# Kernel tuning notes

Hardware: AMD Instinct MI355X
Metric: run time of the kernel (lower is better)

Reference implementation:

```python
import jax, jax.numpy as jnp
import numpy as np

NEG_SLOPE = 0.01  # torch F.leaky_relu default
N_USER = 100000
N_ITEM = 100000
N_EDGE = 640000
D = 128
N_LAYERS = 3  # 1 input + num_hidden_layers(1) + 1 output layer


def setup_inputs() -> dict:
    key = jax.random.key(0)
    ks = jax.random.split(key, 10)
    scale = 1.0 / np.sqrt(D)
    return {
        "h_user": jax.random.normal(ks[0], (N_USER, D), dtype=jnp.float32),
        "h_item": jax.random.normal(ks[1], (N_ITEM, D), dtype=jnp.float32),
        # W[layer, etype] : etype 0 = user-follows->user, 1 = user-clicks->item, 2 = item-clicked_by->user
        "W": jax.random.normal(ks[2], (N_LAYERS, 3, D, D), dtype=jnp.float32) * scale,
        "b": jnp.zeros((N_LAYERS, 3, D), dtype=jnp.float32),
        "follows_src": jax.random.randint(ks[3], (N_EDGE,), 0, N_USER, dtype=jnp.int32),
        "follows_dst": jax.random.randint(ks[4], (N_EDGE,), 0, N_USER, dtype=jnp.int32),
        "clicks_src": jax.random.randint(ks[5], (N_EDGE,), 0, N_USER, dtype=jnp.int32),
        "clicks_dst": jax.random.randint(ks[6], (N_EDGE,), 0, N_ITEM, dtype=jnp.int32),
        "cb_src": jax.random.randint(ks[7], (N_EDGE,), 0, N_ITEM, dtype=jnp.int32),
        "cb_dst": jax.random.randint(ks[8], (N_EDGE,), 0, N_USER, dtype=jnp.int32),
    }


def _etype_conv(h_src, W, b, src, dst, n_dst):
    """Per-etype Linear on src nodes, copy_u gather, mean-aggregate at dst."""
    Wh = h_src @ W + b                     # [N_src, D] dense transform (once per node)
    msg = Wh[src]                          # [E, D] gather
    s = jax.ops.segment_sum(msg, dst, num_segments=n_dst)
    cnt = jax.ops.segment_sum(jnp.ones((src.shape[0],), dtype=Wh.dtype), dst, num_segments=n_dst)
    return s / jnp.maximum(cnt, 1.0)[:, None]  # mean; isolated nodes -> 0


def _rgcn_forward(h_user, h_item, W, b, follows_src, follows_dst,
                  clicks_src, clicks_dst, cb_src, cb_dst):
    hu, hi = h_user, h_item
    for l in range(N_LAYERS):
        # per-etype mean aggregation, then cross-etype 'sum' (DGL multi_update_all)
        agg_u = (_etype_conv(hu, W[l, 0], b[l, 0], follows_src, follows_dst, N_USER)
                 + _etype_conv(hi, W[l, 2], b[l, 2], cb_src, cb_dst, N_USER))
        agg_i = _etype_conv(hu, W[l, 1], b[l, 1], clicks_src, clicks_dst, N_ITEM)
        hu = jax.nn.leaky_relu(agg_u, NEG_SLOPE)
        hi = jax.nn.leaky_relu(agg_i, NEG_SLOPE)
    return jnp.stack([hu, hi])  # [2, 100000, 128]


def reference(h_user, h_item, W, b, follows_src, follows_dst,
              clicks_src, clicks_dst, cb_src, cb_dst):
    return _rgcn_forward(h_user, h_item, W, b, follows_src, follows_dst,
                         clicks_src, clicks_dst, cb_src, cb_dst)
```

## Files before the change

kernel.cpp:

```cpp
#include <hip/hip_runtime.h>

typedef unsigned short u16;
typedef _Float16 f16;
typedef __attribute__((ext_vector_type(4))) _Float16 f16x4;
typedef __attribute__((ext_vector_type(8))) _Float16 f16x8;
typedef __attribute__((ext_vector_type(4))) float f32x4;

#define D 128

__global__ __launch_bounds__(256) void k_pre(
    const float* __restrict__ h_user, const float* __restrict__ h_item,
    const float* __restrict__ W,
    const int* __restrict__ fd, const int* __restrict__ cd,
    const int* __restrict__ cbd,
    u16* __restrict__ h_all, u16* __restrict__ Wtg,
    int* __restrict__ cnt, u16* __restrict__ pos,
    int NU, int NI, int nf, int nc, int ncb, int S,
    int nbCnt, int nbCvtU, int nbCvtI) {
  int b = blockIdx.x;
  if (b < nbCnt) {
    int e = b * 256 + threadIdx.x;
    int d;
    if (e < nf)
      d = fd[e];
    else if (e < nf + nc)
      d = NU + cd[e - nf];
    else if (e < nf + nc + ncb)
      d = NU + NI + cbd[e - nf - nc];
    else
      return;
    int p = atomicAdd(&cnt[d * S], 1);
    pos[e] = (u16)p;
  } else if (b < nbCnt + nbCvtU + nbCvtI) {
    bool isU = b < nbCnt + nbCvtU;
    int i = (b - (isU ? nbCnt : nbCnt + nbCvtU)) * 256 + threadIdx.x;
    int n8 = (isU ? NU : NI) * 16;
    if (i >= n8) return;
    const float4* ip = (const float4*)(isU ? h_user : h_item);
    u16* op = h_all + (isU ? 0 : (size_t)NU * D);
    float4 a = ip[i * 2], c = ip[i * 2 + 1];
    f16x8 v = {(f16)a.x, (f16)a.y, (f16)a.z, (f16)a.w,
               (f16)c.x, (f16)c.y, (f16)c.z, (f16)c.w};
    *(f16x8*)(op + (size_t)i * 8) = v;
  } else {
    int idx = (b - nbCnt - nbCvtU - nbCvtI) * 256 + threadIdx.x;
    if (idx >= 9 * 16384) return;
    int mat = idx >> 14;
    int k = (idx >> 7) & 127;
    int n = idx & 127;
    ((f16*)Wtg)[(size_t)mat * 16384 + n * 128 + k] = (f16)W[idx];
  }
}

__global__ __launch_bounds__(256) void k_scanA(const int* __restrict__ cnt,
                                               int* __restrict__ part, int n, int S) {
  int t = threadIdx.x;
  int idx = blockIdx.x * 1024 + t * 4;
  int s = 0;
#pragma unroll
  for (int j = 0; j < 4; ++j)
    if (idx + j < n) s += cnt[(idx + j) * S];
  for (int off = 1; off < 64; off <<= 1) s += __shfl_down(s, off, 64);
  __shared__ int ws[4];
  if ((t & 63) == 0) ws[t >> 6] = s;
  __syncthreads();
  if (t == 0) part[blockIdx.x] = ws[0] + ws[1] + ws[2] + ws[3];
}

__global__ __launch_bounds__(1024) void k_scanB(int* __restrict__ part, int n_part) {
  __shared__ int sh[1024];
  int t = threadIdx.x;
  int v = (t < n_part) ? part[t] : 0;
  sh[t] = v;
  __syncthreads();
  for (int off = 1; off < 1024; off <<= 1) {
    int u = (t >= off) ? sh[t - off] : 0;
    __syncthreads();
    sh[t] += u;
    __syncthreads();
  }
  if (t < n_part) part[t] = sh[t] - v;
}

__global__ __launch_bounds__(256) void k_scanC(const int* __restrict__ cnt,
                                               const int* __restrict__ part,
                                               int* __restrict__ rs,
                                               int n, int total, int S) {
  int t = threadIdx.x;
  int idx = blockIdx.x * 1024 + t * 4;
  int v0 = 0, v1 = 0, v2 = 0, v3 = 0;
  if (idx < n) v0 = cnt[idx * S];
  if (idx + 1 < n) v1 = cnt[(idx + 1) * S];
  if (idx + 2 < n) v2 = cnt[(idx + 2) * S];
  if (idx + 3 < n) v3 = cnt[(idx + 3) * S];
  int s = v0 + v1 + v2 + v3;
  int inc = s;
  int lane = t & 63, w = t >> 6;
  for (int off = 1; off < 64; off <<= 1) {
    int u = __shfl_up(inc, off, 64);
    if (lane >= off) inc += u;
  }
  __shared__ int ws[4];
  if (lane == 63) ws[w] = inc;
  __syncthreads();
  int woff = 0;
  for (int i = 0; i < w; ++i) woff += ws[i];
  int ex = part[blockIdx.x] + woff + inc - s;
  int4 r;
  r.x = ex;
  r.y = ex + v0;
  r.z = r.y + v1;
  r.w = r.z + v2;
  if (idx + 3 < n)
    *(int4*)(rs + idx) = r;
  else {
    if (idx < n) rs[idx] = r.x;
    if (idx + 1 < n) rs[idx + 1] = r.y;
    if (idx + 2 < n) rs[idx + 2] = r.z;
    if (idx + 3 < n) rs[idx + 3] = r.w;
  }
  if (blockIdx.x == 0 && t == 0) rs[n] = total;
}

__global__ __launch_bounds__(256) void k_fillpos(
    const int* __restrict__ fs, const int* __restrict__ fd,
    const int* __restrict__ cs, const int* __restrict__ cd,
    const int* __restrict__ cbs, const int* __restrict__ cbd,
    const int* __restrict__ rs, const u16* __restrict__ pos,
    int* __restrict__ csr, int NU, int NI, int nf, int nc, int ncb) {
  int e = blockIdx.x * 256 + threadIdx.x;
  int d, s;
  if (e < nf) {
    d = fd[e];
    s = fs[e];
  } else if (e < nf + nc) {
    d = NU + cd[e - nf];
    s = cs[e - nf];
  } else if (e < nf + nc + ncb) {
    d = NU + NI + cbd[e - nf - nc];
    s = cbs[e - nf - nc] + NU;
  } else
    return;
  csr[rs[d] + (int)pos[e]] = s;
}

__global__ __launch_bounds__(256) void k_agg3(
    const u16* __restrict__ h_all, const int* __restrict__ csr,
    const int* __restrict__ rs, u16* __restrict__ M_all, int N3) {
  int wave = (blockIdx.x * 256 + threadIdx.x) >> 6;
  int lane = threadIdx.x & 63;
  int l16 = lane & 15;
  int w = wave * 4 + (lane >> 4);
  bool valid = w < N3;
  int wc = valid ? w : 0;
  int e = rs[wc];
  int en = valid ? rs[wc + 1] : 0;
  int deg = en - e;
  f16x8 acc0 = {0, 0, 0, 0, 0, 0, 0, 0};
  f16x8 acc1 = {0, 0, 0, 0, 0, 0, 0, 0};
  const char* hb = (const char*)h_all;
  unsigned loff = (unsigned)l16 * 16u;

  while (__any(e < en)) {
    bool a0 = e < en, a1 = e + 1 < en, a2 = e + 2 < en, a3 = e + 3 < en;
    bool a4 = e + 4 < en, a5 = e + 5 < en, a6 = e + 6 < en, a7 = e + 7 < en;
    int s0 = a0 ? csr[e] : 0;
    int s1 = a1 ? csr[e + 1] : 0;
    int s2 = a2 ? csr[e + 2] : 0;
    int s3 = a3 ? csr[e + 3] : 0;
    int s4 = a4 ? csr[e + 4] : 0;
    int s5 = a5 ? csr[e + 5] : 0;
    int s6 = a6 ? csr[e + 6] : 0;
    int s7 = a7 ? csr[e + 7] : 0;
    f16x8 v0 = {0, 0, 0, 0, 0, 0, 0, 0}, v1 = {0, 0, 0, 0, 0, 0, 0, 0};
    f16x8 v2 = {0, 0, 0, 0, 0, 0, 0, 0}, v3 = {0, 0, 0, 0, 0, 0, 0, 0};
    f16x8 v4 = {0, 0, 0, 0, 0, 0, 0, 0}, v5 = {0, 0, 0, 0, 0, 0, 0, 0};
    f16x8 v6 = {0, 0, 0, 0, 0, 0, 0, 0}, v7 = {0, 0, 0, 0, 0, 0, 0, 0};
    if (a0) v0 = *(const f16x8*)(hb + ((unsigned)s0 * 256u + loff));
    if (a1) v1 = *(const f16x8*)(hb + ((unsigned)s1 * 256u + loff));
    if (a2) v2 = *(const f16x8*)(hb + ((unsigned)s2 * 256u + loff));
    if (a3) v3 = *(const f16x8*)(hb + ((unsigned)s3 * 256u + loff));
    if (a4) v4 = *(const f16x8*)(hb + ((unsigned)s4 * 256u + loff));
    if (a5) v5 = *(const f16x8*)(hb + ((unsigned)s5 * 256u + loff));
    if (a6) v6 = *(const f16x8*)(hb + ((unsigned)s6 * 256u + loff));
    if (a7) v7 = *(const f16x8*)(hb + ((unsigned)s7 * 256u + loff));
    acc0 += v0;
    acc1 += v1;
    acc0 += v2;
    acc1 += v3;
    acc0 += v4;
    acc1 += v5;
    acc0 += v6;
    acc1 += v7;
    e += 8;
  }

  if (valid) {
    float invf = deg > 0 ? 1.0f / (float)deg : 0.f;
    f16 hinv = (f16)invf;
    f16x8 t = acc0 + acc1;
    f16x8 r = t * hinv;
    *(f16x8*)((char*)M_all + ((unsigned)wc * 256u + loff)) = r;
  }
}

template <int NE, int OUTF32>
__device__ __forceinline__ void gemm_body(
    const u16* __restrict__ mA, const u16* __restrict__ mBp,
    const u16* __restrict__ wtA, const u16* __restrict__ wtB,
    const float* __restrict__ bA, const float* __restrict__ bB,
    const int* __restrict__ rsA, const int* __restrict__ rsB,
    u16* __restrict__ o16, float* __restrict__ o32, int M, int blk) {
  int tid = threadIdx.x, lane = tid & 63, w = tid >> 6;
  int lr = lane & 15;
  int lk = (lane >> 4) * 8;
  long row0 = (long)blk * 128 + w * 32;

  f32x4 acc[2][8];
#pragma unroll
  for (int rt = 0; rt < 2; rt++)
#pragma unroll
    for (int n = 0; n < 8; n++) acc[rt][n] = (f32x4){0.f, 0.f, 0.f, 0.f};

#pragma unroll
  for (int e = 0; e < NE; ++e) {
    const f16* mm = (const f16*)((e == 0) ? mA : mBp);
    const f16* Wg = (const f16*)((e == 0) ? wtA : wtB);
#pragma unroll
    for (int ks = 0; ks < 4; ++ks) {
      int k0 = ks * 32 + lk;
      f16x8 bf[8];
#pragma unroll
      for (int n = 0; n < 8; n++) bf[n] = *(const f16x8*)(Wg + (n * 16 + lr) * D + k0);
#pragma unroll
      for (int rt = 0; rt < 2; rt++) {
        long r = row0 + rt * 16 + lr;
        if (r >= M) r = M - 1;
        f16x8 af = *(const f16x8*)(mm + r * D + k0);
#pragma unroll
        for (int n = 0; n < 8; n++)
          acc[rt][n] = __builtin_amdgcn_mfma_f32_16x16x32_f16(bf[n], af, acc[rt][n], 0, 0, 0);
      }
    }
  }

  int g4 = (lane >> 4) * 4;
  float4 bAr[8], bBr[8];
#pragma unroll
  for (int n = 0; n < 8; n++) {
    bAr[n] = *(const float4*)&bA[n * 16 + g4];
    if (NE == 2) bBr[n] = *(const float4*)&bB[n * 16 + g4];
  }

#pragma unroll
  for (int rt = 0; rt < 2; rt++) {
    long r = row0 + rt * 16 + lr;
    if (r < M) {
      bool mAok = rsA[r + 1] > rsA[r];
      bool mBok = (NE == 2) && (rsB[r + 1] > rsB[r]);
#pragma unroll
      for (int n = 0; n < 8; n++) {
        float4 vv;
        vv.x = acc[rt][n][0];
        vv.y = acc[rt][n][1];
        vv.z = acc[rt][n][2];
        vv.w = acc[rt][n][3];
        if (mAok) {
          vv.x += bAr[n].x;
          vv.y += bAr[n].y;
          vv.z += bAr[n].z;
          vv.w += bAr[n].w;
        }
        if (mBok) {
          vv.x += bBr[n].x;
          vv.y += bBr[n].y;
          vv.z += bBr[n].z;
          vv.w += bBr[n].w;
        }
        vv.x = vv.x > 0.f ? vv.x : 0.01f * vv.x;
        vv.y = vv.y > 0.f ? vv.y : 0.01f * vv.y;
        vv.z = vv.z > 0.f ? vv.z : 0.01f * vv.z;
        vv.w = vv.w > 0.f ? vv.w : 0.01f * vv.w;
        int col = n * 16 + g4;
        if (OUTF32) {
          *(float4*)&o32[r * D + col] = vv;
        } else {
          f16x4 h = {(f16)vv.x, (f16)vv.y, (f16)vv.z, (f16)vv.w};
          *(f16x4*)((f16*)o16 + r * D + col) = h;
        }
      }
    }
  }
}

template <int OUTF32>
__global__ __launch_bounds__(256) void k_gemm2(
    const u16* __restrict__ M_all, const u16* __restrict__ Wl,
    const float* __restrict__ bl, const int* __restrict__ rs_all,
    u16* __restrict__ h_all, float* __restrict__ out,
    int NU, int NI, int nbI) {
  if ((int)blockIdx.x < nbI) {
    gemm_body<1, OUTF32>(M_all + (size_t)NU * D, nullptr,
                         Wl + 16384, nullptr,
                         bl + D, nullptr,
                         rs_all + NU, nullptr,
                         h_all + (size_t)NU * D, out + (size_t)NU * D, NI,
                         blockIdx.x);
  } else {
    gemm_body<2, OUTF32>(M_all, M_all + (size_t)(NU + NI) * D,
                         Wl, Wl + 2 * 16384,
                         bl, bl + 2 * D,
                         rs_all, rs_all + NU + NI,
                         h_all, out, NU, blockIdx.x - nbI);
  }
}

extern "C" void kernel_launch(void* const* d_in, const int* in_sizes, int n_in,
                              void* d_out, int out_size, void* d_ws, size_t ws_size,
                              hipStream_t stream) {
  const float* h_user = (const float*)d_in[0];
  const float* h_item = (const float*)d_in[1];
  const float* W = (const float*)d_in[2];
  const float* bb = (const float*)d_in[3];
  const int* f_src = (const int*)d_in[4];
  const int* f_dst = (const int*)d_in[5];
  const int* c_src = (const int*)d_in[6];
  const int* c_dst = (const int*)d_in[7];
  const int* cb_src = (const int*)d_in[8];
  const int* cb_dst = (const int*)d_in[9];

  const int NU = in_sizes[0] / D;
  const int NI = in_sizes[1] / D;
  const int nEf = in_sizes[4], nEc = in_sizes[6], nEcb = in_sizes[8];
  const int N3 = NU + NI + NU;
  const int nE = nEf + nEc + nEcb;

  size_t fixed = (size_t)(N3 + 1) * 4 + 1024 * 4 + (size_t)9 * 16384 * 2 +
                 (size_t)nE * 4 + (size_t)nE * 2 +
                 (size_t)(NU + NI) * D * 2 + (size_t)N3 * D * 2 + 8192;
  int S = (fixed + (size_t)N3 * 64 <= ws_size) ? 16 : 1;

  char* p = (char*)d_ws;
  auto alloc = [&](size_t bytes) {
    char* r = p;
    p += (bytes + 255) & ~(size_t)255;
    return r;
  };
  int* cnt_pad = (int*)alloc((size_t)N3 * 4 * S);
  int* rs_all = (int*)alloc((size_t)(N3 + 1) * 4);
  int* part = (int*)alloc(1024 * 4);
  u16* Wtg = (u16*)alloc((size_t)9 * 16384 * 2);
  int* csr_all = (int*)alloc((size_t)nE * 4);
  u16* pos = (u16*)alloc((size_t)nE * 2);
  u16* h_all = (u16*)alloc((size_t)(NU + NI) * D * 2);
  u16* M_all = (u16*)alloc((size_t)N3 * D * 2);

  hipMemsetAsync(cnt_pad, 0, (size_t)N3 * 4 * S, stream);

  int nbCnt = (nE + 255) / 256;
  int nbCvtU = (NU * 16 + 255) / 256;
  int nbCvtI = (NI * 16 + 255) / 256;
  int nbW = (9 * 16384 + 255) / 256;
  k_pre<<<nbCnt + nbCvtU + nbCvtI + nbW, 256, 0, stream>>>(
      h_user, h_item, W, f_dst, c_dst, cb_dst, h_all, Wtg, cnt_pad, pos,
      NU, NI, nEf, nEc, nEcb, S, nbCnt, nbCvtU, nbCvtI);

  int n_part = (N3 + 1023) / 1024;
  k_scanA<<<n_part, 256, 0, stream>>>(cnt_pad, part, N3, S);
  k_scanB<<<1, 1024, 0, stream>>>(part, n_part);
  k_scanC<<<n_part, 256, 0, stream>>>(cnt_pad, part, rs_all, N3, nE, S);

  k_fillpos<<<(nE + 255) / 256, 256, 0, stream>>>(f_src, f_dst, c_src, c_dst,
                                                  cb_src, cb_dst, rs_all, pos,
                                                  csr_all, NU, NI, nEf, nEc, nEcb);

  int nbI = (NI + 127) / 128;
  int nbU = (NU + 127) / 128;
  int agg_blocks = ((N3 + 3) / 4 + 3) / 4;

  for (int l = 0; l < 3; ++l) {
    const u16* Wl = Wtg + (size_t)l * 3 * 16384;
    const float* bl = bb + (size_t)l * 3 * D;

    k_agg3<<<agg_blocks, 256, 0, stream>>>(h_all, csr_all, rs_all, M_all, N3);

    if (l < 2)
      k_gemm2<0><<<nbI + nbU, 256, 0, stream>>>(M_all, Wl, bl, rs_all, h_all,
                                                (float*)d_out, NU, NI, nbI);
    else
      k_gemm2<1><<<nbI + nbU, 256, 0, stream>>>(M_all, Wl, bl, rs_all, h_all,
                                                (float*)d_out, NU, NI, nbI);
  }
}
```

Baseline: 565.7 us.

## Pad CSR rows to multiples of four with a zero row to drop predication

Each destination row of the CSR adjacency is padded up to a multiple of four with indices that point at an extra all-zero feature row. This lets the aggregation kernel run unpredicated 8-wide gathers plus one 4-wide tail, and it now reads the true degree from the count array. The prep kernel interleaves the atomic counting blocks with the conversion blocks to spread atomic contention. The count array loses its 16-way stride padding, and per-edge positions shrink to u8 stored in the M_all buffer. In exchange, the kernel gathers extra padded zero rows, adds a padding-fill kernel, and u8 positions assume no node has more than 255 incoming edges per combined row.

```diff
diff --git a/kernel.cpp b/kernel.cpp
--- a/kernel.cpp
+++ b/kernel.cpp
@@ -1,5 +1,6 @@
 #include <hip/hip_runtime.h>
 
+typedef unsigned char u8;
 typedef unsigned short u16;
 typedef _Float16 f16;
 typedef __attribute__((ext_vector_type(4))) _Float16 f16x4;
@@ -7,6 +8,7 @@
 typedef __attribute__((ext_vector_type(4))) float f32x4;
 
 #define D 128
+#define PG 4
 
 __global__ __launch_bounds__(256) void k_pre(
     const float* __restrict__ h_user, const float* __restrict__ h_item,
@@ -14,12 +16,15 @@
     const int* __restrict__ fd, const int* __restrict__ cd,
     const int* __restrict__ cbd,
     u16* __restrict__ h_all, u16* __restrict__ Wtg,
-    int* __restrict__ cnt, u16* __restrict__ pos,
-    int NU, int NI, int nf, int nc, int ncb, int S,
+    int* __restrict__ cnt, u8* __restrict__ pos,
+    int NU, int NI, int nf, int nc, int ncb,
     int nbCnt, int nbCvtU, int nbCvtI) {
   int b = blockIdx.x;
-  if (b < nbCnt) {
-    int e = b * 256 + threadIdx.x;
+  int T = gridDim.x;
+  long before = (long)b * nbCnt / T;
+  long after = (long)(b + 1) * nbCnt / T;
+  if (after > before) {
+    int e = (int)before * 256 + threadIdx.x;
     int d;
     if (e < nf)
       d = fd[e];
@@ -29,37 +34,47 @@
       d = NU + NI + cbd[e - nf - nc];
     else
       return;
-    int p = atomicAdd(&cnt[d * S], 1);
-    pos[e] = (u16)p;
-  } else if (b < nbCnt + nbCvtU + nbCvtI) {
-    bool isU = b < nbCnt + nbCvtU;
-    int i = (b - (isU ? nbCnt : nbCnt + nbCvtU)) * 256 + threadIdx.x;
-    int n8 = (isU ? NU : NI) * 16;
-    if (i >= n8) return;
-    const float4* ip = (const float4*)(isU ? h_user : h_item);
-    u16* op = h_all + (isU ? 0 : (size_t)NU * D);
-    float4 a = ip[i * 2], c = ip[i * 2 + 1];
-    f16x8 v = {(f16)a.x, (f16)a.y, (f16)a.z, (f16)a.w,
-               (f16)c.x, (f16)c.y, (f16)c.z, (f16)c.w};
-    *(f16x8*)(op + (size_t)i * 8) = v;
+    int p = atomicAdd(&cnt[d], 1);
+    pos[e] = (u8)p;
   } else {
-    int idx = (b - nbCnt - nbCvtU - nbCvtI) * 256 + threadIdx.x;
-    if (idx >= 9 * 16384) return;
-    int mat = idx >> 14;
-    int k = (idx >> 7) & 127;
-    int n = idx & 127;
-    ((f16*)Wtg)[(size_t)mat * 16384 + n * 128 + k] = (f16)W[idx];
-  }
-}
+    int v = b - (int)before;
+    if (v < nbCvtU + nbCvtI) {
+      bool isU = v < nbCvtU;
+      int i = (isU ? v : v - nbCvtU) * 256 + threadIdx.x;
+      int n8 = (isU ? NU : NI) * 16;
+      if (i >= n8) return;
+      const float4* ip = (const float4*)(isU ? h_user : h_item);
+      u16* op = h_all + (isU ? 0 : (size_t)NU * D);
+      float4 a = ip[i * 2], c = ip[i * 2 + 1];
+      f16x8 vv = {(f16)a.x, (f16)a.y, (f16)a.z, (f16)a.w,
+                  (f16)c.x, (f16)c.y, (f16)c.z, (f16)c.w};
+      *(f16x8*)(op + (size_t)i * 8) = vv;
+    } else {
+      int idx = (v - nbCvtU - nbCvtI) * 256 + threadIdx.x;
+      if (idx >= 9 * 16384) return;
+      int mat = idx >> 14;
+      int k = (idx >> 7) & 127;
+      int n = idx & 127;
+      ((f16*)Wtg)[(size_t)mat * 16384 + n * 128 + k] = (f16)W[idx];
+    }
+  }
+}
+
+__device__ __forceinline__ int pad4(int x) { return (x + (PG - 1)) & ~(PG - 1); }
 
 __global__ __launch_bounds__(256) void k_scanA(const int* __restrict__ cnt,
-                                               int* __restrict__ part, int n, int S) {
+                                               int* __restrict__ part, int n) {
   int t = threadIdx.x;
   int idx = blockIdx.x * 1024 + t * 4;
   int s = 0;
-#pragma unroll
-  for (int j = 0; j < 4; ++j)
-    if (idx + j < n) s += cnt[(idx + j) * S];
+  if (idx + 3 < n) {
+    int4 c = *(const int4*)(cnt + idx);
+    s = pad4(c.x) + pad4(c.y) + pad4(c.z) + pad4(c.w);
+  } else {
+#pragma unroll
+    for (int j = 0; j < 4; ++j)
+      if (idx + j < n) s += pad4(cnt[idx + j]);
+  }
   for (int off = 1; off < 64; off <<= 1) s += __shfl_down(s, off, 64);
   __shared__ int ws[4];
   if ((t & 63) == 0) ws[t >> 6] = s;
@@ -84,15 +99,22 @@
 
 __global__ __launch_bounds__(256) void k_scanC(const int* __restrict__ cnt,
                                                const int* __restrict__ part,
-                                               int* __restrict__ rs,
-                                               int n, int total, int S) {
+                                               int* __restrict__ rs, int n) {
   int t = threadIdx.x;
   int idx = blockIdx.x * 1024 + t * 4;
   int v0 = 0, v1 = 0, v2 = 0, v3 = 0;
-  if (idx < n) v0 = cnt[idx * S];
-  if (idx + 1 < n) v1 = cnt[(idx + 1) * S];
-  if (idx + 2 < n) v2 = cnt[(idx + 2) * S];
-  if (idx + 3 < n) v3 = cnt[(idx + 3) * S];
+  if (idx + 3 < n) {
+    int4 c = *(const int4*)(cnt + idx);
+    v0 = pad4(c.x);
+    v1 = pad4(c.y);
+    v2 = pad4(c.z);
+    v3 = pad4(c.w);
+  } else {
+    if (idx < n) v0 = pad4(cnt[idx]);
+    if (idx + 1 < n) v1 = pad4(cnt[idx + 1]);
+    if (idx + 2 < n) v2 = pad4(cnt[idx + 2]);
+    if (idx + 3 < n) v3 = pad4(cnt[idx + 3]);
+  }
   int s = v0 + v1 + v2 + v3;
   int inc = s;
   int lane = t & 63, w = t >> 6;
@@ -119,14 +141,31 @@
     if (idx + 2 < n) rs[idx + 2] = r.z;
     if (idx + 3 < n) rs[idx + 3] = r.w;
   }
-  if (blockIdx.x == 0 && t == 0) rs[n] = total;
+  if (idx <= n - 1 && n - 1 < idx + 4) {
+    int j = n - 1 - idx;
+    int incl = (j == 0) ? r.x + v0 : (j == 1) ? r.y + v1 : (j == 2) ? r.z + v2 : r.w + v3;
+    rs[n] = incl;
+  }
+}
+
+__global__ __launch_bounds__(256) void k_padfill(const int* __restrict__ rs,
+                                                 const int* __restrict__ cnt,
+                                                 int* __restrict__ csr, int N3, int ZR) {
+  int d = blockIdx.x * 256 + threadIdx.x;
+  if (d >= N3) return;
+  int deg = cnt[d];
+  int degp = pad4(deg);
+  int base = rs[d] + deg;
+#pragma unroll
+  for (int j = 0; j < PG - 1; ++j)
+    if (j < degp - deg) csr[base + j] = ZR;
 }
 
 __global__ __launch_bounds__(256) void k_fillpos(
     const int* __restrict__ fs, const int* __restrict__ fd,
     const int* __restrict__ cs, const int* __restrict__ cd,
     const int* __restrict__ cbs, const int* __restrict__ cbd,
-    const int* __restrict__ rs, const u16* __restrict__ pos,
+    const int* __restrict__ rs, const u8* __restrict__ pos,
     int* __restrict__ csr, int NU, int NI, int nf, int nc, int ncb) {
   int e = blockIdx.x * 256 + threadIdx.x;
   int d, s;
@@ -146,7 +185,8 @@
 
 __global__ __launch_bounds__(256) void k_agg3(
     const u16* __restrict__ h_all, const int* __restrict__ csr,
-    const int* __restrict__ rs, u16* __restrict__ M_all, int N3) {
+    const int* __restrict__ rs, const int* __restrict__ cnt,
+    u16* __restrict__ M_all, int N3) {
   int wave = (blockIdx.x * 256 + threadIdx.x) >> 6;
   int lane = threadIdx.x & 63;
   int l16 = lane & 15;
@@ -154,36 +194,25 @@
   bool valid = w < N3;
   int wc = valid ? w : 0;
   int e = rs[wc];
-  int en = valid ? rs[wc + 1] : 0;
-  int deg = en - e;
+  int en = valid ? rs[wc + 1] : e;
+  int deg = valid ? cnt[wc] : 0;
   f16x8 acc0 = {0, 0, 0, 0, 0, 0, 0, 0};
   f16x8 acc1 = {0, 0, 0, 0, 0, 0, 0, 0};
   const char* hb = (const char*)h_all;
   unsigned loff = (unsigned)l16 * 16u;
 
-  while (__any(e < en)) {
-    bool a0 = e < en, a1 = e + 1 < en, a2 = e + 2 < en, a3 = e + 3 < en;
-    bool a4 = e + 4 < en, a5 = e + 5 < en, a6 = e + 6 < en, a7 = e + 7 < en;
-    int s0 = a0 ? csr[e] : 0;
-    int s1 = a1 ? csr[e + 1] : 0;
-    int s2 = a2 ? csr[e + 2] : 0;
-    int s3 = a3 ? csr[e + 3] : 0;
-    int s4 = a4 ? csr[e + 4] : 0;
-    int s5 = a5 ? csr[e + 5] : 0;
-    int s6 = a6 ? csr[e + 6] : 0;
-    int s7 = a7 ? csr[e + 7] : 0;
-    f16x8 v0 = {0, 0, 0, 0, 0, 0, 0, 0}, v1 = {0, 0, 0, 0, 0, 0, 0, 0};
-    f16x8 v2 = {0, 0, 0, 0, 0, 0, 0, 0}, v3 = {0, 0, 0, 0, 0, 0, 0, 0};
-    f16x8 v4 = {0, 0, 0, 0, 0, 0, 0, 0}, v5 = {0, 0, 0, 0, 0, 0, 0, 0};
-    f16x8 v6 = {0, 0, 0, 0, 0, 0, 0, 0}, v7 = {0, 0, 0, 0, 0, 0, 0, 0};
-    if (a0) v0 = *(const f16x8*)(hb + ((unsigned)s0 * 256u + loff));
-    if (a1) v1 = *(const f16x8*)(hb + ((unsigned)s1 * 256u + loff));
-    if (a2) v2 = *(const f16x8*)(hb + ((unsigned)s2 * 256u + loff));
-    if (a3) v3 = *(const f16x8*)(hb + ((unsigned)s3 * 256u + loff));
-    if (a4) v4 = *(const f16x8*)(hb + ((unsigned)s4 * 256u + loff));
-    if (a5) v5 = *(const f16x8*)(hb + ((unsigned)s5 * 256u + loff));
-    if (a6) v6 = *(const f16x8*)(hb + ((unsigned)s6 * 256u + loff));
-    if (a7) v7 = *(const f16x8*)(hb + ((unsigned)s7 * 256u + loff));
+  int en8 = e + ((en - e) & ~7);
+  while (e < en8) {
+    int s0 = csr[e], s1 = csr[e + 1], s2 = csr[e + 2], s3 = csr[e + 3];
+    int s4 = csr[e + 4], s5 = csr[e + 5], s6 = csr[e + 6], s7 = csr[e + 7];
+    f16x8 v0 = *(const f16x8*)(hb + ((unsigned)s0 * 256u + loff));
+    f16x8 v1 = *(const f16x8*)(hb + ((unsigned)s1 * 256u + loff));
+    f16x8 v2 = *(const f16x8*)(hb + ((unsigned)s2 * 256u + loff));
+    f16x8 v3 = *(const f16x8*)(hb + ((unsigned)s3 * 256u + loff));
+    f16x8 v4 = *(const f16x8*)(hb + ((unsigned)s4 * 256u + loff));
+    f16x8 v5 = *(const f16x8*)(hb + ((unsigned)s5 * 256u + loff));
+    f16x8 v6 = *(const f16x8*)(hb + ((unsigned)s6 * 256u + loff));
+    f16x8 v7 = *(const f16x8*)(hb + ((unsigned)s7 * 256u + loff));
     acc0 += v0;
     acc1 += v1;
     acc0 += v2;
@@ -193,6 +222,17 @@
     acc0 += v6;
     acc1 += v7;
     e += 8;
+  }
+  if (e < en) {
+    int s0 = csr[e], s1 = csr[e + 1], s2 = csr[e + 2], s3 = csr[e + 3];
+    f16x8 v0 = *(const f16x8*)(hb + ((unsigned)s0 * 256u + loff));
+    f16x8 v1 = *(const f16x8*)(hb + ((unsigned)s1 * 256u + loff));
+    f16x8 v2 = *(const f16x8*)(hb + ((unsigned)s2 * 256u + loff));
+    f16x8 v3 = *(const f16x8*)(hb + ((unsigned)s3 * 256u + loff));
+    acc0 += v0;
+    acc1 += v1;
+    acc0 += v2;
+    acc1 += v3;
   }
 
   if (valid) {
@@ -334,11 +374,7 @@
   const int nEf = in_sizes[4], nEc = in_sizes[6], nEcb = in_sizes[8];
   const int N3 = NU + NI + NU;
   const int nE = nEf + nEc + nEcb;
-
-  size_t fixed = (size_t)(N3 + 1) * 4 + 1024 * 4 + (size_t)9 * 16384 * 2 +
-                 (size_t)nE * 4 + (size_t)nE * 2 +
-                 (size_t)(NU + NI) * D * 2 + (size_t)N3 * D * 2 + 8192;
-  int S = (fixed + (size_t)N3 * 64 <= ws_size) ? 16 : 1;
+  const int ZR = NU + NI;
 
   char* p = (char*)d_ws;
   auto alloc = [&](size_t bytes) {
@@ -346,30 +382,33 @@
     p += (bytes + 255) & ~(size_t)255;
     return r;
   };
-  int* cnt_pad = (int*)alloc((size_t)N3 * 4 * S);
+  int* cnt = (int*)alloc((size_t)N3 * 4);
   int* rs_all = (int*)alloc((size_t)(N3 + 1) * 4);
   int* part = (int*)alloc(1024 * 4);
   u16* Wtg = (u16*)alloc((size_t)9 * 16384 * 2);
-  int* csr_all = (int*)alloc((size_t)nE * 4);
-  u16* pos = (u16*)alloc((size_t)nE * 2);
-  u16* h_all = (u16*)alloc((size_t)(NU + NI) * D * 2);
+  int* csr_all = (int*)alloc(((size_t)nE + (size_t)(PG - 1) * N3) * 4);
+  u16* h_all = (u16*)alloc((size_t)(NU + NI + 1) * D * 2);
   u16* M_all = (u16*)alloc((size_t)N3 * D * 2);
-
-  hipMemsetAsync(cnt_pad, 0, (size_t)N3 * 4 * S, stream);
+  u8* pos = (u8*)M_all;
+  (void)ws_size;
+
+  hipMemsetAsync(cnt, 0, (size_t)N3 * 4, stream);
+  hipMemsetAsync(h_all + (size_t)ZR * D, 0, D * 2, stream);
 
   int nbCnt = (nE + 255) / 256;
   int nbCvtU = (NU * 16 + 255) / 256;
   int nbCvtI = (NI * 16 + 255) / 256;
   int nbW = (9 * 16384 + 255) / 256;
   k_pre<<<nbCnt + nbCvtU + nbCvtI + nbW, 256, 0, stream>>>(
-      h_user, h_item, W, f_dst, c_dst, cb_dst, h_all, Wtg, cnt_pad, pos,
-      NU, NI, nEf, nEc, nEcb, S, nbCnt, nbCvtU, nbCvtI);
+      h_user, h_item, W, f_dst, c_dst, cb_dst, h_all, Wtg, cnt, pos,
+      NU, NI, nEf, nEc, nEcb, nbCnt, nbCvtU, nbCvtI);
 
   int n_part = (N3 + 1023) / 1024;
-  k_scanA<<<n_part, 256, 0, stream>>>(cnt_pad, part, N3, S);
+  k_scanA<<<n_part, 256, 0, stream>>>(cnt, part, N3);
   k_scanB<<<1, 1024, 0, stream>>>(part, n_part);
-  k_scanC<<<n_part, 256, 0, stream>>>(cnt_pad, part, rs_all, N3, nE, S);
-
+  k_scanC<<<n_part, 256, 0, stream>>>(cnt, part, rs_all, N3);
+
+  k_padfill<<<(N3 + 255) / 256, 256, 0, stream>>>(rs_all, cnt, csr_all, N3, ZR);
   k_fillpos<<<(nE + 255) / 256, 256, 0, stream>>>(f_src, f_dst, c_src, c_dst,
                                                   cb_src, cb_dst, rs_all, pos,
                                                   csr_all, NU, NI, nEf, nEc, nEcb);
@@ -382,7 +421,7 @@
     const u16* Wl = Wtg + (size_t)l * 3 * 16384;
     const float* bl = bb + (size_t)l * 3 * D;
 
-    k_agg3<<<agg_blocks, 256, 0, stream>>>(h_all, csr_all, rs_all, M_all, N3);
+    k_agg3<<<agg_blocks, 256, 0, stream>>>(h_all, csr_all, rs_all, cnt, M_all, N3);
 
     if (l < 2)
       k_gemm2<0><<<nbI + nbU, 256, 0, stream>>>(M_all, Wl, bl, rs_all, h_all,
```

After: 549.2 us. 1.03x faster.
